# Kernel tuning notes

Measured on AMD Instinct MI355X. Metric: run time of the kernel, lower is better.

## Reference

```python
import jax, jax.numpy as jnp
import numpy as np

N_NODES = 100000
N_GRAPHS = 512
HID = 128
IN_DIM = 128
OUT_DIM = 10
N_EDGES = 1600000


def gcn_conv(x, src, dst, W, b, n):
    # PyG GCNConv: add self-loops, symmetric normalization D^-1/2 (A+I) D^-1/2, then linear.
    h = x @ W  # [N, H]
    deg = jnp.zeros((n,), h.dtype).at[dst].add(1.0) + 1.0  # +1 self-loop
    dinv = jax.lax.rsqrt(deg)
    norm = dinv[src] * dinv[dst]  # [E]
    agg = jnp.zeros_like(h).at[dst].add(h[src] * norm[:, None])
    agg = agg + h * (dinv * dinv)[:, None]  # self-loop messages
    return agg + b


def setup_inputs() -> dict:
    key = jax.random.key(0)
    ks = jax.random.split(key, 12)
    x = jax.random.normal(ks[0], (N_NODES, IN_DIM), jnp.float32)
    edge_index = jax.random.randint(ks[1], (2, N_EDGES), 0, N_NODES)
    batch = jnp.sort(jax.random.randint(ks[2], (N_NODES,), 0, N_GRAPHS))
    def lin(k, fan_in, shape):
        bound = 1.0 / np.sqrt(fan_in)
        return jax.random.uniform(k, shape, jnp.float32, -bound, bound)
    W1 = lin(ks[3], IN_DIM, (IN_DIM, HID)); b1 = lin(ks[4], IN_DIM, (HID,))
    W2 = lin(ks[5], HID, (HID, HID)); b2 = lin(ks[6], HID, (HID,))
    W3 = lin(ks[7], HID, (HID, HID)); b3 = lin(ks[8], HID, (HID,))
    Wc1 = lin(ks[9], 2 * HID, (2 * HID, HID)); bc1 = lin(ks[9], 2 * HID, (HID,))
    Wc2 = lin(ks[10], HID, (HID, OUT_DIM)); bc2 = lin(ks[11], HID, (OUT_DIM,))
    return {"x": x, "edge_index": edge_index, "batch": batch,
            "W1": W1, "b1": b1, "W2": W2, "b2": b2, "W3": W3, "b3": b3,
            "Wc1": Wc1, "bc1": bc1, "Wc2": Wc2, "bc2": bc2}


def reference(x, edge_index, batch, W1, b1, W2, b2, W3, b3, Wc1, bc1, Wc2, bc2):
    src, dst = edge_index[0], edge_index[1]
    n = x.shape[0]
    h = jax.nn.relu(gcn_conv(x, src, dst, W1, b1, n))
    h = jax.nn.relu(gcn_conv(h, src, dst, W2, b2, n))
    h = gcn_conv(h, src, dst, W3, b3, n)  # no relu after last conv
    # global mean pool
    sums = jax.ops.segment_sum(h, batch, num_segments=N_GRAPHS)
    cnt = jax.ops.segment_sum(jnp.ones((n,), h.dtype), batch, num_segments=N_GRAPHS)
    mean = sums / jnp.maximum(cnt, 1.0)[:, None]
    # global max pool
    mx = jax.ops.segment_max(h, batch, num_segments=N_GRAPHS)
    mx = jnp.where(jnp.isfinite(mx), mx, 0.0)
    g = jnp.concatenate([mean, mx], axis=1)  # [G, 2H]
    g = jax.nn.relu(g @ Wc1 + bc1)
    return g @ Wc2 + bc2
```

## Files before the change

kernel.cpp:

```cpp
#include <hip/hip_runtime.h>

#define H 128
#define CAP 64
#define BCAP 262144

typedef __attribute__((ext_vector_type(8))) short bf16x8;
typedef __attribute__((ext_vector_type(4))) float f32x4;

__device__ __forceinline__ unsigned short f2bf(float f) {
  unsigned u = __float_as_uint(f);
  unsigned r = u + 0x7FFFu + ((u >> 16) & 1u);
  return (unsigned short)(r >> 16);
}
__device__ __forceinline__ float bf2f(unsigned short s) {
  return __uint_as_float(((unsigned)s) << 16);
}

__global__ __launch_bounds__(256) void setup_all(
    const float* __restrict__ x,
    const float* __restrict__ W1, const float* __restrict__ W2, const float* __restrict__ W3,
    unsigned short* __restrict__ Xb, unsigned short* __restrict__ Wt,
    unsigned short* __restrict__ P, unsigned short* __restrict__ Q,
    int* __restrict__ cursor, int cur4, int* __restrict__ bcount,
    int n, int totalX4) {
  long long i = (long long)blockIdx.x * 256 + threadIdx.x;
  if (i < totalX4) {
    float4 v = *(const float4*)(x + i * 4);
    ushort4 o;
    o.x = f2bf(v.x); o.y = f2bf(v.y); o.z = f2bf(v.z); o.w = f2bf(v.w);
    *(ushort4*)(Xb + i * 4) = o;
    return;
  }
  i -= totalX4;
  if (i < 3 * H * H) {
    int w = (int)(i >> 14);
    int rem = (int)i & (H * H - 1);
    int c = rem >> 7;
    int k = rem & 127;
    const float* W = (w == 0) ? W1 : (w == 1) ? W2 : W3;
    Wt[i] = f2bf(W[(size_t)k * H + c]);
    return;
  }
  i -= 3 * H * H;
  if (i < cur4) {
    *(int4*)(cursor + i * 4) = make_int4(0, 0, 0, 0);
    return;
  }
  i -= cur4;
  if (i < H) {
    P[(size_t)n * H + i] = 0;
    Q[(size_t)n * H + i] = 0;
    return;
  }
  i -= H;
  if (i < 8) bcount[i] = 0;
}

__global__ __launch_bounds__(256) void bucket_edges(
    const int* __restrict__ src, const int* __restrict__ dst,
    int2* __restrict__ buckets, int* __restrict__ bcount,
    int ne, float invr) {
  __shared__ int cnt[8];
  __shared__ int gbase[8];
  int tid = threadIdx.x;
  if (tid < 8) cnt[tid] = 0;
  __syncthreads();

  int ne4 = ne >> 2;
  int e4 = blockIdx.x * 256 + tid;
  bool valid = e4 < ne4;
  int4 s4, d4;
  int r0 = 0, r1 = 0, r2 = 0, r3 = 0;
  int l0 = 0, l1 = 0, l2 = 0, l3 = 0;
  if (valid) {
    s4 = *(const int4*)(src + e4 * 4);
    d4 = *(const int4*)(dst + e4 * 4);
    int t;
    t = (int)((float)d4.x * invr); r0 = t < 0 ? 0 : (t > 7 ? 7 : t);
    t = (int)((float)d4.y * invr); r1 = t < 0 ? 0 : (t > 7 ? 7 : t);
    t = (int)((float)d4.z * invr); r2 = t < 0 ? 0 : (t > 7 ? 7 : t);
    t = (int)((float)d4.w * invr); r3 = t < 0 ? 0 : (t > 7 ? 7 : t);
    l0 = atomicAdd(&cnt[r0], 1);
    l1 = atomicAdd(&cnt[r1], 1);
    l2 = atomicAdd(&cnt[r2], 1);
    l3 = atomicAdd(&cnt[r3], 1);
  }
  __syncthreads();
  if (tid < 8) gbase[tid] = atomicAdd(&bcount[tid], cnt[tid]);
  __syncthreads();
  if (valid) {
    int p0 = gbase[r0] + l0;
    int p1 = gbase[r1] + l1;
    int p2 = gbase[r2] + l2;
    int p3 = gbase[r3] + l3;
    if (p0 < BCAP) buckets[(r0 << 18) + p0] = make_int2(s4.x, d4.x);
    if (p1 < BCAP) buckets[(r1 << 18) + p1] = make_int2(s4.y, d4.y);
    if (p2 < BCAP) buckets[(r2 << 18) + p2] = make_int2(s4.z, d4.z);
    if (p3 < BCAP) buckets[(r3 << 18) + p3] = make_int2(s4.w, d4.w);
  }
  if (blockIdx.x == 0 && tid < (ne & 3)) {
    int e = ne4 * 4 + tid;
    int d = dst[e];
    int t = (int)((float)d * invr);
    int rr = t < 0 ? 0 : (t > 7 ? 7 : t);
    int p = atomicAdd(&bcount[rr], 1);
    if (p < BCAP) buckets[(rr << 18) + p] = make_int2(src[e], d);
  }
}

__global__ __launch_bounds__(256) void place_edges(
    const int2* __restrict__ buckets, const int* __restrict__ bcount,
    int* __restrict__ cursor, int* __restrict__ csr_src, int slices) {
  int r = blockIdx.x & 7;
  int s = blockIdx.x >> 3;
  int cnt = bcount[r]; if (cnt > BCAP) cnt = BCAP;
  int chunk = (cnt + slices - 1) / slices;
  int beg = s * chunk;
  int end = beg + chunk; if (end > cnt) end = cnt;
  const int2* b = buckets + ((size_t)r << 18);
  for (int i = beg + threadIdx.x; i < end; i += 256) {
    int2 e = b[i];
    int p = atomicAdd(&cursor[e.y], 1);
    if (p < CAP) csr_src[(size_t)e.y * CAP + p] = e.x;
  }
}

__global__ void dinv_gstart(const int* __restrict__ deg, float* __restrict__ dinv,
                            const int* __restrict__ batch, int* __restrict__ g_start,
                            int n, int G) {
  int i = blockIdx.x * blockDim.x + threadIdx.x;
  if (i >= n) return;
  dinv[i] = rsqrtf((float)(deg[i] + 1));
  int b = batch[i];
  int prev = (i == 0) ? -1 : batch[i - 1];
  for (int g = prev + 1; g <= b; ++g) g_start[g] = i;
  if (i == n - 1) {
    for (int g = b + 1; g <= G; ++g) g_start[g] = n;
  }
}

#define SWLD 136
__global__ __launch_bounds__(256) void gemm_mfma(
    const unsigned short* __restrict__ Ab, const unsigned short* __restrict__ Wt,
    const float* __restrict__ dinv, unsigned short* __restrict__ outb, int n) {
  __shared__ unsigned short sW[H * SWLD];
  int tid = threadIdx.x;
  {
    int c = tid >> 1, hh = tid & 1;
    const int4* s = (const int4*)(Wt + (size_t)c * H + hh * 64);
    int4* d = (int4*)(sW + (size_t)c * SWLD + hh * 64);
#pragma unroll
    for (int i = 0; i < 8; ++i) d[i] = s[i];
  }
  __syncthreads();

  int wave = tid >> 6;
  int lane = tid & 63;
  int m = lane & 15;
  int quad = lane >> 4;
  int row = blockIdx.x * 64 + wave * 16 + m;
  bool rv = row < n;

  f32x4 acc[8];
#pragma unroll
  for (int t = 0; t < 8; ++t) acc[t] = (f32x4){0.f, 0.f, 0.f, 0.f};

  const unsigned short* arow = Ab + (size_t)(rv ? row : 0) * H;
#pragma unroll
  for (int k0 = 0; k0 < H; k0 += 32) {
    bf16x8 af;
    if (rv) af = *(const bf16x8*)(arow + k0 + quad * 8);
    else    af = (bf16x8){0, 0, 0, 0, 0, 0, 0, 0};
#pragma unroll
    for (int ct = 0; ct < 8; ++ct) {
      bf16x8 bfr = *(const bf16x8*)(sW + (size_t)(ct * 16 + m) * SWLD + k0 + quad * 8);
      acc[ct] = __builtin_amdgcn_mfma_f32_16x16x32_bf16(af, bfr, acc[ct], 0, 0, 0);
    }
  }

  int orow0 = blockIdx.x * 64 + wave * 16 + quad * 4;
#pragma unroll
  for (int r = 0; r < 4; ++r) {
    int orow = orow0 + r;
    if (orow < n) {
      float dv = dinv[orow];
      unsigned short* o = outb + (size_t)orow * H + m;
#pragma unroll
      for (int ct = 0; ct < 8; ++ct) o[ct * 16] = f2bf(acc[ct][r] * dv);
    }
  }
}

template <bool RELU, bool OUTF32>
__global__ __launch_bounds__(256) void aggregate_bf(
    const unsigned short* __restrict__ hs, const int* __restrict__ deg_,
    const int* __restrict__ csr_src, const float* __restrict__ dinv,
    const float* __restrict__ b, void* __restrict__ outv, int n) {
  int node = blockIdx.x * 8 + (threadIdx.x >> 5);
  if (node >= n) return;
  int c = (threadIdx.x & 31) << 2;
  int deg = deg_[node]; if (deg > CAP) deg = CAP;
  int beg = node * CAP;
  int end = beg + ((deg + 7) & ~7);

  ushort4 sv = *(const ushort4*)(hs + (size_t)node * H + c);
  float4 acc;
  acc.x = bf2f(sv.x); acc.y = bf2f(sv.y); acc.z = bf2f(sv.z); acc.w = bf2f(sv.w);

  int4 ia, ib;
  if (beg < end) {
    ia = *(const int4*)(csr_src + beg);
    ib = *(const int4*)(csr_src + beg + 4);
  }
  for (int k = beg; k < end; k += 8) {
    int4 ca = ia, cb = ib;
    int kn = k + 8;
    if (kn < end) {
      ia = *(const int4*)(csr_src + kn);
      ib = *(const int4*)(csr_src + kn + 4);
    }
    int rk = k - beg;
    if (rk + 8 > deg) {
      ca.x = (rk + 0 < deg) ? ca.x : n;
      ca.y = (rk + 1 < deg) ? ca.y : n;
      ca.z = (rk + 2 < deg) ? ca.z : n;
      ca.w = (rk + 3 < deg) ? ca.w : n;
      cb.x = (rk + 4 < deg) ? cb.x : n;
      cb.y = (rk + 5 < deg) ? cb.y : n;
      cb.z = (rk + 6 < deg) ? cb.z : n;
      cb.w = (rk + 7 < deg) ? cb.w : n;
    }
    ushort4 v0 = *(const ushort4*)(hs + (size_t)ca.x * H + c);
    ushort4 v1 = *(const ushort4*)(hs + (size_t)ca.y * H + c);
    ushort4 v2 = *(const ushort4*)(hs + (size_t)ca.z * H + c);
    ushort4 v3 = *(const ushort4*)(hs + (size_t)ca.w * H + c);
    ushort4 v4 = *(const ushort4*)(hs + (size_t)cb.x * H + c);
    ushort4 v5 = *(const ushort4*)(hs + (size_t)cb.y * H + c);
    ushort4 v6 = *(const ushort4*)(hs + (size_t)cb.z * H + c);
    ushort4 v7 = *(const ushort4*)(hs + (size_t)cb.w * H + c);
    acc.x += ((bf2f(v0.x) + bf2f(v1.x)) + (bf2f(v2.x) + bf2f(v3.x))) +
             ((bf2f(v4.x) + bf2f(v5.x)) + (bf2f(v6.x) + bf2f(v7.x)));
    acc.y += ((bf2f(v0.y) + bf2f(v1.y)) + (bf2f(v2.y) + bf2f(v3.y))) +
             ((bf2f(v4.y) + bf2f(v5.y)) + (bf2f(v6.y) + bf2f(v7.y)));
    acc.z += ((bf2f(v0.z) + bf2f(v1.z)) + (bf2f(v2.z) + bf2f(v3.z))) +
             ((bf2f(v4.z) + bf2f(v5.z)) + (bf2f(v6.z) + bf2f(v7.z)));
    acc.w += ((bf2f(v0.w) + bf2f(v1.w)) + (bf2f(v2.w) + bf2f(v3.w))) +
             ((bf2f(v4.w) + bf2f(v5.w)) + (bf2f(v6.w) + bf2f(v7.w)));
  }

  float dv = dinv[node];
  float4 bb = *(const float4*)(b + c);
  float4 o;
  o.x = fmaf(acc.x, dv, bb.x);
  o.y = fmaf(acc.y, dv, bb.y);
  o.z = fmaf(acc.z, dv, bb.z);
  o.w = fmaf(acc.w, dv, bb.w);
  if (RELU) {
    o.x = fmaxf(o.x, 0.f); o.y = fmaxf(o.y, 0.f);
    o.z = fmaxf(o.z, 0.f); o.w = fmaxf(o.w, 0.f);
  }
  if (OUTF32) {
    *(float4*)((float*)outv + (size_t)node * H + c) = o;
  } else {
    ushort4 ob;
    ob.x = f2bf(o.x); ob.y = f2bf(o.y); ob.z = f2bf(o.z); ob.w = f2bf(o.w);
    *(ushort4*)((unsigned short*)outv + (size_t)node * H + c) = ob;
  }
}

__global__ __launch_bounds__(256) void pool2(
    const float* __restrict__ h, const int* __restrict__ g_start,
    float* __restrict__ gmean, float* __restrict__ gmax, int n) {
  __shared__ float ssum[16][64];
  __shared__ float smax[16][64];
  int g = blockIdx.x >> 1;
  int half = blockIdx.x & 1;
  int beg = g_start[g];
  int end = g_start[g + 1];
  int q = threadIdx.x >> 4;
  int c = (threadIdx.x & 15) << 2;
  int cg = half * 64 + c;

  float4 s = make_float4(0.f, 0.f, 0.f, 0.f);
  float4 m = make_float4(-INFINITY, -INFINITY, -INFINITY, -INFINITY);
  for (int node = beg + q; node < end; node += 16) {
    float4 v = *(const float4*)(h + (size_t)node * H + cg);
    s.x += v.x; s.y += v.y; s.z += v.z; s.w += v.w;
    m.x = fmaxf(m.x, v.x); m.y = fmaxf(m.y, v.y);
    m.z = fmaxf(m.z, v.z); m.w = fmaxf(m.w, v.w);
  }
  *(float4*)&ssum[q][c] = s;
  *(float4*)&smax[q][c] = m;
  __syncthreads();

  int cnt = end - beg;
  int t = threadIdx.x;
  if (t < 64) {
    float tot = 0.f;
#pragma unroll
    for (int qq = 0; qq < 16; ++qq) tot += ssum[qq][t];
    gmean[(size_t)g * H + half * 64 + t] = tot / fmaxf((float)cnt, 1.0f);
  } else if (t < 128) {
    int cc = t - 64;
    float mx = -INFINITY;
#pragma unroll
    for (int qq = 0; qq < 16; ++qq) mx = fmaxf(mx, smax[qq][cc]);
    gmax[(size_t)g * H + half * 64 + cc] = (cnt == 0) ? 0.0f : mx;
  }
}

__global__ __launch_bounds__(128) void classify_kernel(
    const float* __restrict__ gmean, const float* __restrict__ gmax,
    const float* __restrict__ Wc1, const float* __restrict__ bc1,
    const float* __restrict__ Wc2, const float* __restrict__ bc2,
    float* __restrict__ out) {
  __shared__ float gv[2 * H];
  __shared__ float hid[H];
  int gid = blockIdx.x;
  int t = threadIdx.x;
  gv[t] = gmean[(size_t)gid * H + t];
  gv[H + t] = gmax[(size_t)gid * H + t];
  __syncthreads();
  float acc = 0.f;
#pragma unroll 8
  for (int k = 0; k < 2 * H; ++k) acc = fmaf(gv[k], Wc1[(size_t)k * H + t], acc);
  hid[t] = fmaxf(acc + bc1[t], 0.f);
  __syncthreads();
  if (t < 10) {
    float a2 = 0.f;
    for (int j = 0; j < H; ++j) a2 = fmaf(hid[j], Wc2[(size_t)j * 10 + t], a2);
    out[(size_t)gid * 10 + t] = a2 + bc2[t];
  }
}

extern "C" void kernel_launch(void* const* d_in, const int* in_sizes, int n_in,
                              void* d_out, int out_size, void* d_ws, size_t ws_size,
                              hipStream_t stream) {
  const float* x    = (const float*)d_in[0];
  const int* ei     = (const int*)d_in[1];
  const int* batch  = (const int*)d_in[2];
  const float* W1   = (const float*)d_in[3];
  const float* b1   = (const float*)d_in[4];
  const float* W2   = (const float*)d_in[5];
  const float* b2   = (const float*)d_in[6];
  const float* W3   = (const float*)d_in[7];
  const float* b3   = (const float*)d_in[8];
  const float* Wc1  = (const float*)d_in[9];
  const float* bc1  = (const float*)d_in[10];
  const float* Wc2  = (const float*)d_in[11];
  const float* bc2  = (const float*)d_in[12];
  float* out = (float*)d_out;

  const int n  = in_sizes[2];
  const int ne = in_sizes[1] / 2;
  const int G  = 512;
  const size_t NFb = (size_t)(n + 1) * H;

  const int* src = ei;
  const int* dst = ei + ne;

  unsigned short* P_bf = (unsigned short*)d_ws;
  unsigned short* Q_bf = P_bf + NFb;
  float*          F2f  = (float*)(Q_bf + NFb);
  unsigned short* Xb   = (unsigned short*)F2f;
  int* csr_src = (int*)(F2f + (size_t)n * H);
  const size_t csr_cap = (size_t)n * CAP;
  char* p = (char*)(csr_src + csr_cap);
  int*            cursor   = (int*)p;            p += (size_t)n * 4;
  float*          dinv     = (float*)p;          p += (size_t)n * 4;
  int*            g_start  = (int*)p;            p += (size_t)(G + 1) * 4;
  float*          gmean    = (float*)p;          p += (size_t)G * H * 4;
  float*          gmax     = (float*)p;          p += (size_t)G * H * 4;
  p = (char*)(((uintptr_t)p + 255) & ~(uintptr_t)255);
  unsigned short* Wt       = (unsigned short*)p; p += (size_t)3 * H * H * 2;
  int*            bcount   = (int*)p;            p += 32;
  int2*           buckets  = (int2*)Q_bf;

  {
    int totalX4 = n * H / 4;
    int cur4 = n / 4;
    long long tot = (long long)totalX4 + 3 * H * H + cur4 + H + 8;
    int blocks = (int)((tot + 255) / 256);
    setup_all<<<blocks, 256, 0, stream>>>(x, W1, W2, W3, Xb, Wt,
                                          P_bf, Q_bf, cursor, cur4, bcount, n, totalX4);
  }

  int range = (n + 7) / 8;
  float invr = 1.0f / (float)range;
  int bblocks = (ne / 4 + 255) / 256;
  bucket_edges<<<bblocks, 256, 0, stream>>>(src, dst, buckets, bcount, ne, invr);
  place_edges<<<8 * 256, 256, 0, stream>>>(buckets, bcount, cursor, csr_src, 256);
  dinv_gstart<<<(n + 255) / 256, 256, 0, stream>>>(cursor, dinv, batch, g_start, n, G);

  const int tile_grid = (n + 63) / 64;
  const int node_grid = (n + 7) / 8;

  gemm_mfma<<<tile_grid, 256, 0, stream>>>(Xb, Wt, dinv, Q_bf, n);
  aggregate_bf<true, false><<<node_grid, 256, 0, stream>>>(Q_bf, cursor, csr_src, dinv, b1, P_bf, n);

  gemm_mfma<<<tile_grid, 256, 0, stream>>>(P_bf, Wt + H * H, dinv, Q_bf, n);
  aggregate_bf<true, false><<<node_grid, 256, 0, stream>>>(Q_bf, cursor, csr_src, dinv, b2, P_bf, n);

  gemm_mfma<<<tile_grid, 256, 0, stream>>>(P_bf, Wt + 2 * H * H, dinv, Q_bf, n);
  aggregate_bf<false, true><<<node_grid, 256, 0, stream>>>(Q_bf, cursor, csr_src, dinv, b3, F2f, n);

  pool2<<<2 * G, 256, 0, stream>>>(F2f, g_start, gmean, gmax, n);
  classify_kernel<<<G, 128, 0, stream>>>(gmean, gmax, Wc1, bc1, Wc2, bc2, out);
}
```

Baseline: 471.6 us.

## Build CSR via fine-grained 256-node buckets with shared-memory per-node cursors

Replaces the 8-way coarse edge bucketing and the global-atomic placement pass with a two-stage split. Edges are first partitioned into 256-node buckets using block-local histograms, then one block per bucket assigns CSR slots through shared-memory counters and writes degree and dinv directly. This removes the global per-node atomics, the cursor zeroing, and the separate dinv/g_start kernel, whose g_start work is folded into setup. Buckets are capped at 6144 edges, so an unusually dense 256-node range would silently drop edges.

```diff
diff --git a/kernel.cpp b/kernel.cpp
--- a/kernel.cpp
+++ b/kernel.cpp
@@ -2,7 +2,9 @@
 
 #define H 128
 #define CAP 64
-#define BCAP 262144
+#define NB 256
+#define BPCAP 6144
+#define EPB 8192
 
 typedef __attribute__((ext_vector_type(8))) short bf16x8;
 typedef __attribute__((ext_vector_type(4))) float f32x4;
@@ -20,8 +22,9 @@
     const float* __restrict__ x,
     const float* __restrict__ W1, const float* __restrict__ W2, const float* __restrict__ W3,
     unsigned short* __restrict__ Xb, unsigned short* __restrict__ Wt,
+    const int* __restrict__ batch, int* __restrict__ g_start, int G,
     unsigned short* __restrict__ P, unsigned short* __restrict__ Q,
-    int* __restrict__ cursor, int cur4, int* __restrict__ bcount,
+    int* __restrict__ bcount,
     int n, int totalX4) {
   long long i = (long long)blockIdx.x * 256 + threadIdx.x;
   if (i < totalX4) {
@@ -42,100 +45,82 @@
     return;
   }
   i -= 3 * H * H;
-  if (i < cur4) {
-    *(int4*)(cursor + i * 4) = make_int4(0, 0, 0, 0);
+  if (i < n) {
+    int ii = (int)i;
+    int b = batch[ii];
+    int prev = (ii == 0) ? -1 : batch[ii - 1];
+    for (int g = prev + 1; g <= b; ++g) g_start[g] = ii;
+    if (ii == n - 1) {
+      for (int g = b + 1; g <= G; ++g) g_start[g] = n;
+    }
     return;
   }
-  i -= cur4;
+  i -= n;
   if (i < H) {
     P[(size_t)n * H + i] = 0;
     Q[(size_t)n * H + i] = 0;
     return;
   }
   i -= H;
-  if (i < 8) bcount[i] = 0;
-}
-
-__global__ __launch_bounds__(256) void bucket_edges(
+  if (i < 512) bcount[i] = 0;
+}
+
+__global__ __launch_bounds__(256) void split1(
     const int* __restrict__ src, const int* __restrict__ dst,
     int2* __restrict__ buckets, int* __restrict__ bcount,
-    int ne, float invr) {
-  __shared__ int cnt[8];
-  __shared__ int gbase[8];
+    int ne, int nbuck) {
+  __shared__ int cnt[512];
+  __shared__ int gbase[512];
   int tid = threadIdx.x;
-  if (tid < 8) cnt[tid] = 0;
-  __syncthreads();
-
-  int ne4 = ne >> 2;
-  int e4 = blockIdx.x * 256 + tid;
-  bool valid = e4 < ne4;
-  int4 s4, d4;
-  int r0 = 0, r1 = 0, r2 = 0, r3 = 0;
-  int l0 = 0, l1 = 0, l2 = 0, l3 = 0;
-  if (valid) {
-    s4 = *(const int4*)(src + e4 * 4);
-    d4 = *(const int4*)(dst + e4 * 4);
-    int t;
-    t = (int)((float)d4.x * invr); r0 = t < 0 ? 0 : (t > 7 ? 7 : t);
-    t = (int)((float)d4.y * invr); r1 = t < 0 ? 0 : (t > 7 ? 7 : t);
-    t = (int)((float)d4.z * invr); r2 = t < 0 ? 0 : (t > 7 ? 7 : t);
-    t = (int)((float)d4.w * invr); r3 = t < 0 ? 0 : (t > 7 ? 7 : t);
-    l0 = atomicAdd(&cnt[r0], 1);
-    l1 = atomicAdd(&cnt[r1], 1);
-    l2 = atomicAdd(&cnt[r2], 1);
-    l3 = atomicAdd(&cnt[r3], 1);
-  }
-  __syncthreads();
-  if (tid < 8) gbase[tid] = atomicAdd(&bcount[tid], cnt[tid]);
-  __syncthreads();
-  if (valid) {
-    int p0 = gbase[r0] + l0;
-    int p1 = gbase[r1] + l1;
-    int p2 = gbase[r2] + l2;
-    int p3 = gbase[r3] + l3;
-    if (p0 < BCAP) buckets[(r0 << 18) + p0] = make_int2(s4.x, d4.x);
-    if (p1 < BCAP) buckets[(r1 << 18) + p1] = make_int2(s4.y, d4.y);
-    if (p2 < BCAP) buckets[(r2 << 18) + p2] = make_int2(s4.z, d4.z);
-    if (p3 < BCAP) buckets[(r3 << 18) + p3] = make_int2(s4.w, d4.w);
-  }
-  if (blockIdx.x == 0 && tid < (ne & 3)) {
-    int e = ne4 * 4 + tid;
+  for (int i = tid; i < 512; i += 256) cnt[i] = 0;
+  __syncthreads();
+
+  int beg = blockIdx.x * EPB;
+  int end = beg + EPB; if (end > ne) end = ne;
+
+  for (int e = beg + tid; e < end; e += 256) {
     int d = dst[e];
-    int t = (int)((float)d * invr);
-    int rr = t < 0 ? 0 : (t > 7 ? 7 : t);
-    int p = atomicAdd(&bcount[rr], 1);
-    if (p < BCAP) buckets[(rr << 18) + p] = make_int2(src[e], d);
-  }
-}
-
-__global__ __launch_bounds__(256) void place_edges(
+    atomicAdd(&cnt[d >> 8], 1);
+  }
+  __syncthreads();
+  for (int i = tid; i < nbuck; i += 256) {
+    int c = cnt[i];
+    gbase[i] = (c > 0) ? atomicAdd(&bcount[i], c) : 0;
+    cnt[i] = 0;
+  }
+  __syncthreads();
+  for (int e = beg + tid; e < end; e += 256) {
+    int s = src[e];
+    int d = dst[e];
+    int b = d >> 8;
+    int l = atomicAdd(&cnt[b], 1);
+    int pos = gbase[b] + l;
+    if (pos < BPCAP) buckets[(size_t)b * BPCAP + pos] = make_int2(s, d);
+  }
+}
+
+__global__ __launch_bounds__(256) void build_csr(
     const int2* __restrict__ buckets, const int* __restrict__ bcount,
-    int* __restrict__ cursor, int* __restrict__ csr_src, int slices) {
-  int r = blockIdx.x & 7;
-  int s = blockIdx.x >> 3;
-  int cnt = bcount[r]; if (cnt > BCAP) cnt = BCAP;
-  int chunk = (cnt + slices - 1) / slices;
-  int beg = s * chunk;
-  int end = beg + chunk; if (end > cnt) end = cnt;
-  const int2* b = buckets + ((size_t)r << 18);
-  for (int i = beg + threadIdx.x; i < end; i += 256) {
-    int2 e = b[i];
-    int p = atomicAdd(&cursor[e.y], 1);
-    if (p < CAP) csr_src[(size_t)e.y * CAP + p] = e.x;
-  }
-}
-
-__global__ void dinv_gstart(const int* __restrict__ deg, float* __restrict__ dinv,
-                            const int* __restrict__ batch, int* __restrict__ g_start,
-                            int n, int G) {
-  int i = blockIdx.x * blockDim.x + threadIdx.x;
-  if (i >= n) return;
-  dinv[i] = rsqrtf((float)(deg[i] + 1));
-  int b = batch[i];
-  int prev = (i == 0) ? -1 : batch[i - 1];
-  for (int g = prev + 1; g <= b; ++g) g_start[g] = i;
-  if (i == n - 1) {
-    for (int g = b + 1; g <= G; ++g) g_start[g] = n;
+    int* __restrict__ csr_src, int* __restrict__ deg, float* __restrict__ dinv,
+    int n) {
+  __shared__ int cur[NB];
+  int b = blockIdx.x;
+  int tid = threadIdx.x;
+  cur[tid] = 0;
+  __syncthreads();
+  int cntb = bcount[b]; if (cntb > BPCAP) cntb = BPCAP;
+  const int2* bp = buckets + (size_t)b * BPCAP;
+  for (int i = tid; i < cntb; i += 256) {
+    int2 e = bp[i];
+    int slot = atomicAdd(&cur[e.y & (NB - 1)], 1);
+    if (slot < CAP) csr_src[(size_t)e.y * CAP + slot] = e.x;
+  }
+  __syncthreads();
+  int node = b * NB + tid;
+  if (node < n) {
+    int d = cur[tid];
+    deg[node] = d;
+    dinv[node] = rsqrtf((float)(d + 1));
   }
 }
 
@@ -366,43 +351,41 @@
   int* csr_src = (int*)(F2f + (size_t)n * H);
   const size_t csr_cap = (size_t)n * CAP;
   char* p = (char*)(csr_src + csr_cap);
-  int*            cursor   = (int*)p;            p += (size_t)n * 4;
+  int*            deg      = (int*)p;            p += (size_t)n * 4;
   float*          dinv     = (float*)p;          p += (size_t)n * 4;
   int*            g_start  = (int*)p;            p += (size_t)(G + 1) * 4;
   float*          gmean    = (float*)p;          p += (size_t)G * H * 4;
   float*          gmax     = (float*)p;          p += (size_t)G * H * 4;
   p = (char*)(((uintptr_t)p + 255) & ~(uintptr_t)255);
   unsigned short* Wt       = (unsigned short*)p; p += (size_t)3 * H * H * 2;
-  int*            bcount   = (int*)p;            p += 32;
+  int*            bcount   = (int*)p;            p += 512 * 4;
   int2*           buckets  = (int2*)Q_bf;
+
+  const int nbuck = (n + NB - 1) / NB;
 
   {
     int totalX4 = n * H / 4;
-    int cur4 = n / 4;
-    long long tot = (long long)totalX4 + 3 * H * H + cur4 + H + 8;
+    long long tot = (long long)totalX4 + 3 * H * H + n + H + 512;
     int blocks = (int)((tot + 255) / 256);
     setup_all<<<blocks, 256, 0, stream>>>(x, W1, W2, W3, Xb, Wt,
-                                          P_bf, Q_bf, cursor, cur4, bcount, n, totalX4);
-  }
-
-  int range = (n + 7) / 8;
-  float invr = 1.0f / (float)range;
-  int bblocks = (ne / 4 + 255) / 256;
-  bucket_edges<<<bblocks, 256, 0, stream>>>(src, dst, buckets, bcount, ne, invr);
-  place_edges<<<8 * 256, 256, 0, stream>>>(buckets, bcount, cursor, csr_src, 256);
-  dinv_gstart<<<(n + 255) / 256, 256, 0, stream>>>(cursor, dinv, batch, g_start, n, G);
+                                          batch, g_start, G,
+                                          P_bf, Q_bf, bcount, n, totalX4);
+  }
+
+  split1<<<(ne + EPB - 1) / EPB, 256, 0, stream>>>(src, dst, buckets, bcount, ne, nbuck);
+  build_csr<<<nbuck, 256, 0, stream>>>(buckets, bcount, csr_src, deg, dinv, n);
 
   const int tile_grid = (n + 63) / 64;
   const int node_grid = (n + 7) / 8;
 
   gemm_mfma<<<tile_grid, 256, 0, stream>>>(Xb, Wt, dinv, Q_bf, n);
-  aggregate_bf<true, false><<<node_grid, 256, 0, stream>>>(Q_bf, cursor, csr_src, dinv, b1, P_bf, n);
+  aggregate_bf<true, false><<<node_grid, 256, 0, stream>>>(Q_bf, deg, csr_src, dinv, b1, P_bf, n);
 
   gemm_mfma<<<tile_grid, 256, 0, stream>>>(P_bf, Wt + H * H, dinv, Q_bf, n);
-  aggregate_bf<true, false><<<node_grid, 256, 0, stream>>>(Q_bf, cursor, csr_src, dinv, b2, P_bf, n);
+  aggregate_bf<true, false><<<node_grid, 256, 0, stream>>>(Q_bf, deg, csr_src, dinv, b2, P_bf, n);
 
   gemm_mfma<<<tile_grid, 256, 0, stream>>>(P_bf, Wt + 2 * H * H, dinv, Q_bf, n);
-  aggregate_bf<false, true><<<node_grid, 256, 0, stream>>>(Q_bf, cursor, csr_src, dinv, b3, F2f, n);
+  aggregate_bf<false, true><<<node_grid, 256, 0, stream>>>(Q_bf, deg, csr_src, dinv, b3, F2f, n);
 
   pool2<<<2 * G, 256, 0, stream>>>(F2f, g_start, gmean, gmax, n);
   classify_kernel<<<G, 128, 0, stream>>>(gmean, gmax, Wc1, bc1, Wc2, bc2, out);
```

New measurement: 432.0 us. 1.09x faster.
